# Optimization experiments

Measured on AMD Instinct MI355X. Metric: run time of the kernel, lower is better.

## Reference

```python
import jax, jax.numpy as jnp
import numpy as np

B, N, E = 8, 10000, 160000
D_IN, D_H = 128, 128
EPS = 1e-5


def setup_inputs() -> dict:
    key = jax.random.key(0)
    ks = jax.random.split(key, 10)
    x = jax.random.normal(ks[0], (B, N, D_IN), dtype=jnp.float32)
    h_prev = jax.random.normal(ks[1], (B, N, D_H), dtype=jnp.float32)
    edge_index = jax.random.randint(ks[2], (2, E), 0, N, dtype=jnp.int32)
    d_cat = D_IN + D_H
    s = 1.0 / np.sqrt(d_cat)
    def w(k):
        return jax.random.uniform(k, (d_cat, D_H), jnp.float32, -s, s)
    def b(k):
        return jax.random.uniform(k, (D_H,), jnp.float32, -s, s)
    return {
        "x": x, "edge_index": edge_index, "h_prev": h_prev,
        "Wz": w(ks[3]), "bz": b(ks[4]),
        "Wr": w(ks[5]), "br": b(ks[6]),
        "Wc": w(ks[7]), "bc": b(ks[8]),
        "gamma": jnp.ones((D_H,), jnp.float32),
        "beta": jnp.zeros((D_H,), jnp.float32),
    }


def _gcn(x, W, bias, src, dst, norm, n_nodes):
    # PyG GCNConv: linear transform, gather from src, weight by sym-norm, scatter-add to dst
    msg = (x @ W)[src] * norm[:, None]          # [E_total, D_H]
    return jax.ops.segment_sum(msg, dst, num_segments=n_nodes) + bias


def reference(x, edge_index, h_prev, Wz, bz, Wr, br, Wc, bc, gamma, beta):
    Bx, Nx, _ = x.shape
    BN = Bx * Nx
    x_flat = x.reshape(BN, -1)
    h_flat = h_prev.reshape(BN, -1)

    # batch the edge index with per-graph node offsets (all edges are in-range)
    offsets = (jnp.arange(Bx, dtype=edge_index.dtype) * Nx)[:, None]
    src = (edge_index[0][None, :] + offsets).reshape(-1)
    dst = (edge_index[1][None, :] + offsets).reshape(-1)

    # GCN self-loops + symmetric normalization (shared by all three convs)
    loops = jnp.arange(BN, dtype=src.dtype)
    src = jnp.concatenate([src, loops])
    dst = jnp.concatenate([dst, loops])
    deg = jax.ops.segment_sum(jnp.ones_like(dst, dtype=x.dtype), dst, num_segments=BN)
    dis = jnp.where(deg > 0, 1.0 / jnp.sqrt(jnp.maximum(deg, 1.0)), 0.0)
    norm = dis[src] * dis[dst]

    xh = jnp.concatenate([x_flat, h_flat], axis=1)
    z = jax.nn.sigmoid(_gcn(xh, Wz, bz, src, dst, norm, BN))
    r = jax.nn.sigmoid(_gcn(xh, Wr, br, src, dst, norm, BN))
    xrh = jnp.concatenate([x_flat, r * h_flat], axis=1)
    h_cand = jnp.tanh(_gcn(xrh, Wc, bc, src, dst, norm, BN))

    h_new = (1.0 - z) * h_flat + z * h_cand

    # LayerNorm over last dim
    mu = h_new.mean(axis=-1, keepdims=True)
    var = ((h_new - mu) ** 2).mean(axis=-1, keepdims=True)
    h_new = (h_new - mu) / jnp.sqrt(var + EPS) * gamma + beta
    return h_new.reshape(Bx, Nx, -1)
```

## Files before the change

kernel.cpp:

```cpp
#include <hip/hip_runtime.h>

#define NN 10000
#define BB 8
#define EE 160000
#define DH 128
#define LN_EPS 1e-5f

typedef unsigned short ushort_t;
typedef unsigned int uint_t;

typedef __bf16 bf16x8 __attribute__((ext_vector_type(8)));
typedef float floatx4 __attribute__((ext_vector_type(4)));

__device__ __forceinline__ float b2f(uint_t u) { return __uint_as_float(u << 16); }
__device__ __forceinline__ ushort_t f2b(float f) {
    uint_t u = __float_as_uint(f);
    return (ushort_t)((u + 0x7fffu + ((u >> 16) & 1u)) >> 16);
}
__device__ __forceinline__ uint_t pack2(float lo, float hi) {
    return (uint_t)f2b(lo) | ((uint_t)f2b(hi) << 16);
}
__device__ __forceinline__ float sigm(float x) { return 1.0f / (1.0f + __expf(-x)); }
__device__ __forceinline__ float tanh_fast(float x) {
    float ex = __expf(2.0f * x);
    return 1.0f - 2.0f / (ex + 1.0f);
}
__device__ __forceinline__ void acc8(float* a, float w, uint4 v) {
    a[0] += w * __uint_as_float(v.x << 16);
    a[1] += w * __uint_as_float(v.x & 0xffff0000u);
    a[2] += w * __uint_as_float(v.y << 16);
    a[3] += w * __uint_as_float(v.y & 0xffff0000u);
    a[4] += w * __uint_as_float(v.z << 16);
    a[5] += w * __uint_as_float(v.z & 0xffff0000u);
    a[6] += w * __uint_as_float(v.w << 16);
    a[7] += w * __uint_as_float(v.w & 0xffff0000u);
}


__global__ void count_deg(const int* __restrict__ ei, int* __restrict__ cnt) {
    int e = blockIdx.x * 256 + threadIdx.x;
    if (e < EE) atomicAdd(&cnt[ei[EE + e]], 1);
}

__global__ __launch_bounds__(256) void scan1(const int* __restrict__ cnt,
                                             int* __restrict__ offs,
                                             int* __restrict__ bsum) {
    __shared__ int s[256];
    const int t = threadIdx.x, idx = blockIdx.x * 256 + t;
    int x = (idx < NN) ? cnt[idx] : 0;
    s[t] = x;
    __syncthreads();
    for (int o = 1; o < 256; o <<= 1) {
        int v = s[t];
        int u = (t >= o) ? s[t - o] : 0;
        __syncthreads();
        s[t] = v + u;
        __syncthreads();
    }
    if (idx < NN) offs[idx] = s[t] - x;
    if (t == 255) bsum[blockIdx.x] = s[255];
}

__global__ __launch_bounds__(64) void scan2(int* __restrict__ bsum, int* __restrict__ offs) {
    __shared__ int sb[40];
    const int t = threadIdx.x;
    if (t < 40) sb[t] = bsum[t];
    __syncthreads();
    if (t == 0) {
        int acc = 0;
        for (int i = 0; i < 40; ++i) {
            int v = sb[i];
            sb[i] = acc;
            acc += v;
        }
        offs[NN] = EE;
    }
    __syncthreads();
    if (t < 40) bsum[t] = sb[t];
}

__global__ __launch_bounds__(256) void scan3(const int* __restrict__ cnt,
                                             const int* __restrict__ bsum,
                                             int* __restrict__ offs,
                                             int* __restrict__ cursor,
                                             float* __restrict__ dis) {
    const int idx = blockIdx.x * 256 + threadIdx.x;
    if (idx < NN) {
        int off = offs[idx] + bsum[blockIdx.x];
        offs[idx] = off;
        cursor[idx] = off;
        dis[idx] = rsqrtf((float)(cnt[idx] + 1));
    }
}

__global__ void fill_csr(const int* __restrict__ ei, int* __restrict__ cursor,
                         const float* __restrict__ dis, int* __restrict__ csr_src,
                         ushort_t* __restrict__ csr_w) {
    int e = blockIdx.x * 256 + threadIdx.x;
    if (e < EE) {
        int s = ei[e];
        int d = ei[EE + e];
        int pos = atomicAdd(&cursor[d], 1);
        csr_src[pos] = s;
        csr_w[pos] = f2b(dis[s]);
    }
}


__global__ __launch_bounds__(256) void packwt_k(const float* __restrict__ x,
                                                const float* __restrict__ h,
                                                ushort_t* __restrict__ xb,
                                                ushort_t* __restrict__ hb,
                                                const float* __restrict__ Wz,
                                                const float* __restrict__ Wr,
                                                const float* __restrict__ Wc,
                                                ushort_t* __restrict__ Wt_zr,
                                                ushort_t* __restrict__ Wt_c) {
    if (blockIdx.x < 10000) {
        const size_t o = ((size_t)blockIdx.x * 256 + threadIdx.x) * 4;
        float4 vx = *(const float4*)(x + o);
        uint2 px;
        px.x = pack2(vx.x, vx.y);
        px.y = pack2(vx.z, vx.w);
        *(uint2*)(xb + o) = px;
        float4 vh = *(const float4*)(h + o);
        uint2 ph;
        ph.x = pack2(vh.x, vh.y);
        ph.y = pack2(vh.z, vh.w);
        *(uint2*)(hb + o) = ph;
    } else {
        const int col = blockIdx.x - 10000, k = threadIdx.x;
        if (col < 256) {
            float v = (col < 128) ? Wz[(size_t)k * 128 + col]
                                  : Wr[(size_t)k * 128 + col - 128];
            Wt_zr[(size_t)col * 256 + k] = f2b(v);
        } else {
            int c2 = col - 256;
            Wt_c[(size_t)c2 * 256 + k] = f2b(Wc[(size_t)k * 128 + c2]);
        }
    }
}


template <int NB>
__global__ __launch_bounds__(256) void gather4(
    const ushort_t* __restrict__ src0, const ushort_t* __restrict__ src1,
    const int* __restrict__ offs, const int* __restrict__ csr_src,
    const ushort_t* __restrict__ csr_w, const float* __restrict__ dis,
    ushort_t* __restrict__ dst0, ushort_t* __restrict__ dst1) {
    const int tid = threadIdx.x, lane = tid & 63;
    const int b = blockIdx.x & 7;
    const int n = (blockIdx.x >> 3) * 4 + (tid >> 6);
    const int g = lane >> 4, il = lane & 15;
    const ushort_t* base0 = src0 + (size_t)b * NN * 128;
    const ushort_t* base1 = (NB == 2) ? (src1 + (size_t)b * NN * 128) : base0;

    float a0[8], a1[8];
#pragma unroll
    for (int j = 0; j < 8; ++j) {
        a0[j] = 0.f;
        a1[j] = 0.f;
    }

    const float dn = dis[n];
    if (g == 0) {
        const uint_t off = (uint_t)n * 128u + (uint_t)il * 8u;
        uint4 v = *(const uint4*)(base0 + off);
        acc8(a0, dn, v);
        if (NB == 2) {
            uint4 vv = *(const uint4*)(base1 + off);
            acc8(a1, dn, vv);
        }
    }

    const int e0 = offs[n], e1 = offs[n + 1];
    for (int ch = e0; ch < e1; ch += 64) {
        const int rem = e1 - ch;
        int idx = 0, wb = 0;
        if (lane < rem) {
            idx = csr_src[ch + lane];
            wb = (int)((uint_t)csr_w[ch + lane] << 16);
        }
        const int m = rem < 64 ? rem : 64;
        const int groups = (m + 3) >> 2;
        int pidx = g * 4;
#pragma unroll 2
        for (int i = 0; i < groups; ++i) {
            const int s = __builtin_amdgcn_ds_bpermute(pidx, idx);
            const float w =
                __uint_as_float((uint_t)__builtin_amdgcn_ds_bpermute(pidx, wb));
            pidx += 16;
            const uint_t off = (uint_t)s * 128u + (uint_t)il * 8u;
            uint4 v = *(const uint4*)(base0 + off);
            acc8(a0, w, v);
            if (NB == 2) {
                uint4 vv = *(const uint4*)(base1 + off);
                acc8(a1, w, vv);
            }
        }
    }

#pragma unroll
    for (int j = 0; j < 8; ++j) {
        a0[j] *= dn;
        a0[j] += __shfl_xor(a0[j], 16);
        a0[j] += __shfl_xor(a0[j], 32);
    }
    if (NB == 2) {
#pragma unroll
        for (int j = 0; j < 8; ++j) {
            a1[j] *= dn;
            a1[j] += __shfl_xor(a1[j], 16);
            a1[j] += __shfl_xor(a1[j], 32);
        }
    }

    if (lane < 16) {
        const size_t o = ((size_t)b * NN + n) * 128 + (size_t)il * 8;
        uint4 st;
        st.x = pack2(a0[0], a0[1]);
        st.y = pack2(a0[2], a0[3]);
        st.z = pack2(a0[4], a0[5]);
        st.w = pack2(a0[6], a0[7]);
        *(uint4*)(dst0 + o) = st;
        if (NB == 2) {
            uint4 st1;
            st1.x = pack2(a1[0], a1[1]);
            st1.y = pack2(a1[2], a1[3]);
            st1.z = pack2(a1[4], a1[5]);
            st1.w = pack2(a1[6], a1[7]);
            *(uint4*)(dst1 + o) = st1;
        }
    }
}


template <int PHASE>
__global__ __launch_bounds__(256) void gemm_k(
    const ushort_t* __restrict__ A1, const ushort_t* __restrict__ A2,
    const ushort_t* __restrict__ Wt, const float* __restrict__ bz,
    const float* __restrict__ br, const float* __restrict__ bc,
    const float* __restrict__ h_prev, const ushort_t* __restrict__ z_in,
    const float* __restrict__ gamma, const float* __restrict__ beta,
    ushort_t* __restrict__ z_out, ushort_t* __restrict__ rh_out,
    float* __restrict__ f_out) {
    __shared__ __align__(16) ushort_t As[128 * 72];
    __shared__ __align__(16) ushort_t Bs[128 * 72];
    const int tid = threadIdx.x;
    const int rb0 = blockIdx.x * 128;
    const int mode = (PHASE == 1) ? 2 : blockIdx.y;
    const int cb0 = (mode == 1) ? 128 : 0;

    const int wv = tid >> 6, lane = tid & 63;
    const int l15 = lane & 15, q = lane >> 4;
    const int sr = tid >> 1;
    const int kh = (tid & 1) * 32;

    floatx4 acc[2][8];
#pragma unroll
    for (int i = 0; i < 2; ++i)
#pragma unroll
        for (int j = 0; j < 8; ++j) acc[i][j] = (floatx4){0.f, 0.f, 0.f, 0.f};

    for (int k0 = 0; k0 < 256; k0 += 64) {
        {
            const int kg = k0 + kh;
            const ushort_t* s = (kg < 128) ? (A1 + (size_t)(rb0 + sr) * 128 + kg)
                                           : (A2 + (size_t)(rb0 + sr) * 128 + (kg - 128));
            ushort_t* dst = &As[sr * 72 + kh];
#pragma unroll
            for (int i = 0; i < 4; ++i) *(uint4*)(dst + i * 8) = *(const uint4*)(s + i * 8);
        }
        {
            const ushort_t* s = Wt + (size_t)(cb0 + sr) * 256 + k0 + kh;
            ushort_t* dst = &Bs[sr * 72 + kh];
#pragma unroll
            for (int i = 0; i < 4; ++i) *(uint4*)(dst + i * 8) = *(const uint4*)(s + i * 8);
        }
        __syncthreads();
#pragma unroll
        for (int ks = 0; ks < 2; ++ks) {
            const int ko = ks * 32 + q * 8;
            bf16x8 a0 = *(const bf16x8*)&As[(wv * 32 + l15) * 72 + ko];
            bf16x8 a1 = *(const bf16x8*)&As[(wv * 32 + 16 + l15) * 72 + ko];
#pragma unroll
            for (int j = 0; j < 8; ++j) {
                bf16x8 b = *(const bf16x8*)&Bs[(j * 16 + l15) * 72 + ko];
                acc[0][j] = __builtin_amdgcn_mfma_f32_16x16x32_bf16(a0, b, acc[0][j], 0, 0, 0);
                acc[1][j] = __builtin_amdgcn_mfma_f32_16x16x32_bf16(a1, b, acc[1][j], 0, 0, 0);
            }
        }
        __syncthreads();
    }

    if (mode == 0) {
        float bv[8];
#pragma unroll
        for (int j = 0; j < 8; ++j) bv[j] = bz[j * 16 + l15];
#pragma unroll
        for (int i = 0; i < 2; ++i)
#pragma unroll
            for (int j = 0; j < 8; ++j)
#pragma unroll
                for (int v = 0; v < 4; ++v) {
                    int row = rb0 + wv * 32 + i * 16 + q * 4 + v;
                    z_out[(size_t)row * 128 + j * 16 + l15] = f2b(sigm(acc[i][j][v] + bv[j]));
                }
    } else if (mode == 1) {
        float bv[8];
#pragma unroll
        for (int j = 0; j < 8; ++j) bv[j] = br[j * 16 + l15];
#pragma unroll
        for (int i = 0; i < 2; ++i)
#pragma unroll
            for (int j = 0; j < 8; ++j)
#pragma unroll
                for (int v = 0; v < 4; ++v) {
                    int row = rb0 + wv * 32 + i * 16 + q * 4 + v;
                    float r = sigm(acc[i][j][v] + bv[j]);
                    float hh = h_prev[(size_t)row * 128 + j * 16 + l15];
                    rh_out[(size_t)row * 128 + j * 16 + l15] = f2b(r * hh);
                }
    } else {
        float bv[8], gv[8], bev[8];
#pragma unroll
        for (int j = 0; j < 8; ++j) {
            bv[j] = bc[j * 16 + l15];
            gv[j] = gamma[j * 16 + l15];
            bev[j] = beta[j * 16 + l15];
        }
#pragma unroll
        for (int i = 0; i < 2; ++i)
#pragma unroll
            for (int v = 0; v < 4; ++v) {
                const int row = rb0 + wv * 32 + i * 16 + q * 4 + v;
                float hn[8];
                float s = 0.f;
#pragma unroll
                for (int j = 0; j < 8; ++j) {
                    float hc = tanh_fast(acc[i][j][v] + bv[j]);
                    float zz = b2f((uint_t)z_in[(size_t)row * 128 + j * 16 + l15]);
                    float hh = h_prev[(size_t)row * 128 + j * 16 + l15];
                    hn[j] = (1.0f - zz) * hh + zz * hc;
                    s += hn[j];
                }
#pragma unroll
                for (int o = 8; o > 0; o >>= 1) s += __shfl_xor(s, o);
                float mu = s * (1.0f / 128.0f);
                float vv = 0.f;
#pragma unroll
                for (int j = 0; j < 8; ++j) {
                    float d = hn[j] - mu;
                    vv += d * d;
                }
#pragma unroll
                for (int o = 8; o > 0; o >>= 1) vv += __shfl_xor(vv, o);
                float inv = rsqrtf(vv * (1.0f / 128.0f) + LN_EPS);
#pragma unroll
                for (int j = 0; j < 8; ++j)
                    f_out[(size_t)row * 128 + j * 16 + l15] =
                        (hn[j] - mu) * inv * gv[j] + bev[j];
            }
    }
}


extern "C" void kernel_launch(void* const* d_in, const int* in_sizes, int n_in,
                              void* d_out, int out_size, void* d_ws, size_t ws_size,
                              hipStream_t stream) {
    const float* x = (const float*)d_in[0];
    const int* ei = (const int*)d_in[1];
    const float* h = (const float*)d_in[2];
    const float* Wz = (const float*)d_in[3];
    const float* bz = (const float*)d_in[4];
    const float* Wr = (const float*)d_in[5];
    const float* br = (const float*)d_in[6];
    const float* Wc = (const float*)d_in[7];
    const float* bcv = (const float*)d_in[8];
    const float* gamma = (const float*)d_in[9];
    const float* beta = (const float*)d_in[10];
    float* out = (float*)d_out;

    char* w = (char*)d_ws;
    int* offs = (int*)(w + 0);
    float* dis = (float*)(w + 40960);
    int* csr_src = (int*)(w + 81920);
    ushort_t* csr_w = (ushort_t*)(w + 721920);
    ushort_t* Wt_zr = (ushort_t*)(w + 1041920);
    ushort_t* Wt_c = (ushort_t*)(w + 1172992);
    ushort_t* xb = (ushort_t*)(w + 1239040);
    ushort_t* hb = (ushort_t*)(w + 21719040);
    ushort_t* agg_x = (ushort_t*)(w + 42199040);
    ushort_t* agg_h = (ushort_t*)(w + 62679040);
    int* cnt = (int*)(w + 1239040);
    int* cursor = (int*)(w + 1280000);
    int* bsum = (int*)(w + 1320000);
    ushort_t* z_buf = xb;
    ushort_t* rh_bf = hb;
    ushort_t* agg_rh = agg_h;

    hipMemsetAsync(cnt, 0, NN * sizeof(int), stream);
    count_deg<<<EE / 256, 256, 0, stream>>>(ei, cnt);
    scan1<<<40, 256, 0, stream>>>(cnt, offs, bsum);
    scan2<<<1, 64, 0, stream>>>(bsum, offs);
    scan3<<<40, 256, 0, stream>>>(cnt, bsum, offs, cursor, dis);
    fill_csr<<<EE / 256, 256, 0, stream>>>(ei, cursor, dis, csr_src, csr_w);
    packwt_k<<<10384, 256, 0, stream>>>(x, h, xb, hb, Wz, Wr, Wc, Wt_zr, Wt_c);

    gather4<2><<<(BB * NN) / 4, 256, 0, stream>>>(xb, hb, offs, csr_src, csr_w, dis,
                                                  agg_x, agg_h);
    gemm_k<0><<<dim3(80000 / 128, 2), 256, 0, stream>>>(
        agg_x, agg_h, Wt_zr, bz, br, bcv, h, (const ushort_t*)0, gamma, beta,
        z_buf, rh_bf, (float*)0);
    gather4<1><<<(BB * NN) / 4, 256, 0, stream>>>(rh_bf, (const ushort_t*)0, offs,
                                                  csr_src, csr_w, dis, agg_rh,
                                                  (ushort_t*)0);
    gemm_k<1><<<dim3(80000 / 128, 1), 256, 0, stream>>>(
        agg_x, agg_rh, Wt_c, bz, br, bcv, h, z_buf, gamma, beta,
        (ushort_t*)0, (ushort_t*)0, out);
}
```

Baseline: 332.7 us.

## Process all batch graphs per wavefront in gather, broadcasting edges via readlane

The gather kernel now assigns one node to each wavefront across all 8 batch graphs, not one node per graph. Each 16-lane group handles two batch slices, so CSR indices and weights are loaded once and shared by all batches. Edges are broadcast with readlane in a scalar loop, which removes the ds_bpermute calls and the cross-lane shuffle reduction at the end. The grid is 8x smaller and each thread holds more accumulators, which adds register pressure and gives fewer waves to hide memory latency.

```diff
diff --git a/kernel.cpp b/kernel.cpp
--- a/kernel.cpp
+++ b/kernel.cpp
@@ -143,33 +143,35 @@
 
 
 template <int NB>
-__global__ __launch_bounds__(256) void gather4(
+__global__ __launch_bounds__(256) void gatherB(
     const ushort_t* __restrict__ src0, const ushort_t* __restrict__ src1,
     const int* __restrict__ offs, const int* __restrict__ csr_src,
     const ushort_t* __restrict__ csr_w, const float* __restrict__ dis,
     ushort_t* __restrict__ dst0, ushort_t* __restrict__ dst1) {
     const int tid = threadIdx.x, lane = tid & 63;
-    const int b = blockIdx.x & 7;
-    const int n = (blockIdx.x >> 3) * 4 + (tid >> 6);
+    const int n = __builtin_amdgcn_readfirstlane((blockIdx.x << 2) + (tid >> 6));
     const int g = lane >> 4, il = lane & 15;
-    const ushort_t* base0 = src0 + (size_t)b * NN * 128;
-    const ushort_t* base1 = (NB == 2) ? (src1 + (size_t)b * NN * 128) : base0;
-
-    float a0[8], a1[8];
+    const uint_t lo0 = (uint_t)g * (NN * 128u) + (uint_t)il * 8u;
+    const uint_t lo1 = lo0 + 4u * NN * 128u;
+
+    float ax0[8], ax1[8], ah0[8], ah1[8];
 #pragma unroll
     for (int j = 0; j < 8; ++j) {
-        a0[j] = 0.f;
-        a1[j] = 0.f;
+        ax0[j] = 0.f;
+        ax1[j] = 0.f;
+        ah0[j] = 0.f;
+        ah1[j] = 0.f;
     }
 
     const float dn = dis[n];
-    if (g == 0) {
-        const uint_t off = (uint_t)n * 128u + (uint_t)il * 8u;
-        uint4 v = *(const uint4*)(base0 + off);
-        acc8(a0, dn, v);
+    {
+        const ushort_t* r0 = src0 + (size_t)n * 128;
+        acc8(ax0, dn, *(const uint4*)(r0 + lo0));
+        acc8(ax1, dn, *(const uint4*)(r0 + lo1));
         if (NB == 2) {
-            uint4 vv = *(const uint4*)(base1 + off);
-            acc8(a1, dn, vv);
+            const ushort_t* r1 = src1 + (size_t)n * 128;
+            acc8(ah0, dn, *(const uint4*)(r1 + lo0));
+            acc8(ah1, dn, *(const uint4*)(r1 + lo1));
         }
     }
 
@@ -182,55 +184,45 @@
             wb = (int)((uint_t)csr_w[ch + lane] << 16);
         }
         const int m = rem < 64 ? rem : 64;
-        const int groups = (m + 3) >> 2;
-        int pidx = g * 4;
-#pragma unroll 2
-        for (int i = 0; i < groups; ++i) {
-            const int s = __builtin_amdgcn_ds_bpermute(pidx, idx);
-            const float w =
-                __uint_as_float((uint_t)__builtin_amdgcn_ds_bpermute(pidx, wb));
-            pidx += 16;
-            const uint_t off = (uint_t)s * 128u + (uint_t)il * 8u;
-            uint4 v = *(const uint4*)(base0 + off);
-            acc8(a0, w, v);
+#pragma unroll 4
+        for (int i = 0; i < m; ++i) {
+            const int s = __builtin_amdgcn_readlane(idx, i);
+            const float w = __uint_as_float((uint_t)__builtin_amdgcn_readlane(wb, i));
+            const ushort_t* r0 = src0 + (size_t)s * 128;
+            acc8(ax0, w, *(const uint4*)(r0 + lo0));
+            acc8(ax1, w, *(const uint4*)(r0 + lo1));
             if (NB == 2) {
-                uint4 vv = *(const uint4*)(base1 + off);
-                acc8(a1, w, vv);
+                const ushort_t* r1 = src1 + (size_t)s * 128;
+                acc8(ah0, w, *(const uint4*)(r1 + lo0));
+                acc8(ah1, w, *(const uint4*)(r1 + lo1));
             }
         }
     }
 
-#pragma unroll
-    for (int j = 0; j < 8; ++j) {
-        a0[j] *= dn;
-        a0[j] += __shfl_xor(a0[j], 16);
-        a0[j] += __shfl_xor(a0[j], 32);
-    }
+    const size_t ob0 = ((size_t)g * NN + n) * 128 + (size_t)il * 8;
+    const size_t ob1 = ob0 + (size_t)4 * NN * 128;
+    uint4 st;
+    st.x = pack2(ax0[0] * dn, ax0[1] * dn);
+    st.y = pack2(ax0[2] * dn, ax0[3] * dn);
+    st.z = pack2(ax0[4] * dn, ax0[5] * dn);
+    st.w = pack2(ax0[6] * dn, ax0[7] * dn);
+    *(uint4*)(dst0 + ob0) = st;
+    st.x = pack2(ax1[0] * dn, ax1[1] * dn);
+    st.y = pack2(ax1[2] * dn, ax1[3] * dn);
+    st.z = pack2(ax1[4] * dn, ax1[5] * dn);
+    st.w = pack2(ax1[6] * dn, ax1[7] * dn);
+    *(uint4*)(dst0 + ob1) = st;
     if (NB == 2) {
-#pragma unroll
-        for (int j = 0; j < 8; ++j) {
-            a1[j] *= dn;
-            a1[j] += __shfl_xor(a1[j], 16);
-            a1[j] += __shfl_xor(a1[j], 32);
-        }
-    }
-
-    if (lane < 16) {
-        const size_t o = ((size_t)b * NN + n) * 128 + (size_t)il * 8;
-        uint4 st;
-        st.x = pack2(a0[0], a0[1]);
-        st.y = pack2(a0[2], a0[3]);
-        st.z = pack2(a0[4], a0[5]);
-        st.w = pack2(a0[6], a0[7]);
-        *(uint4*)(dst0 + o) = st;
-        if (NB == 2) {
-            uint4 st1;
-            st1.x = pack2(a1[0], a1[1]);
-            st1.y = pack2(a1[2], a1[3]);
-            st1.z = pack2(a1[4], a1[5]);
-            st1.w = pack2(a1[6], a1[7]);
-            *(uint4*)(dst1 + o) = st1;
-        }
+        st.x = pack2(ah0[0] * dn, ah0[1] * dn);
+        st.y = pack2(ah0[2] * dn, ah0[3] * dn);
+        st.z = pack2(ah0[4] * dn, ah0[5] * dn);
+        st.w = pack2(ah0[6] * dn, ah0[7] * dn);
+        *(uint4*)(dst1 + ob0) = st;
+        st.x = pack2(ah1[0] * dn, ah1[1] * dn);
+        st.y = pack2(ah1[2] * dn, ah1[3] * dn);
+        st.z = pack2(ah1[4] * dn, ah1[5] * dn);
+        st.w = pack2(ah1[6] * dn, ah1[7] * dn);
+        *(uint4*)(dst1 + ob1) = st;
     }
 }
 
@@ -407,14 +399,14 @@
     fill_csr<<<EE / 256, 256, 0, stream>>>(ei, cursor, dis, csr_src, csr_w);
     packwt_k<<<10384, 256, 0, stream>>>(x, h, xb, hb, Wz, Wr, Wc, Wt_zr, Wt_c);
 
-    gather4<2><<<(BB * NN) / 4, 256, 0, stream>>>(xb, hb, offs, csr_src, csr_w, dis,
-                                                  agg_x, agg_h);
+    gatherB<2><<<NN / 4, 256, 0, stream>>>(xb, hb, offs, csr_src, csr_w, dis,
+                                           agg_x, agg_h);
     gemm_k<0><<<dim3(80000 / 128, 2), 256, 0, stream>>>(
         agg_x, agg_h, Wt_zr, bz, br, bcv, h, (const ushort_t*)0, gamma, beta,
         z_buf, rh_bf, (float*)0);
-    gather4<1><<<(BB * NN) / 4, 256, 0, stream>>>(rh_bf, (const ushort_t*)0, offs,
-                                                  csr_src, csr_w, dis, agg_rh,
-                                                  (ushort_t*)0);
+    gatherB<1><<<NN / 4, 256, 0, stream>>>(rh_bf, (const ushort_t*)0, offs,
+                                           csr_src, csr_w, dis, agg_rh,
+                                           (ushort_t*)0);
     gemm_k<1><<<dim3(80000 / 128, 1), 256, 0, stream>>>(
         agg_x, agg_rh, Wt_c, bz, br, bcv, h, z_buf, gamma, beta,
         (ushort_t*)0, (ushort_t*)0, out);
```

Result: slower. 383.5 us (+15.3%).
